# Kernel tuning notes

Measured on AMD Instinct MI355X. Metric: run time of the kernel, lower is better.

## Reference

```python
import jax, jax.numpy as jnp
import numpy as np

T, NP, NA, NV = 8, 16000, 16000, 200
DIN, H, KA, L = 256, 256, 4, 5
YEARS_TRAIN = (5, 6, 7)
BETA, EPS = 0.5, 1.0
SQRT2 = 1.4142135623730951


def setup_inputs() -> dict:
    key = jax.random.key(0)
    ks = jax.random.split(key, 24)
    s = 0.05
    return {
        'x_paper': jax.random.normal(ks[0], (T, NP, DIN), jnp.float32),
        'x_author': jax.random.normal(ks[1], (T, NA, DIN), jnp.float32),
        'x_venue': jax.random.normal(ks[2], (T, NV, DIN), jnp.float32),
        'neigh_author_idx': jax.random.randint(ks[3], (NP, KA), 0, NA),
        'neigh_venue_idx': jax.random.randint(ks[4], (NP,), 0, NV),
        'y_true': jax.random.uniform(ks[5], (len(YEARS_TRAIN), NP, L), jnp.float32, 0.0, 50.0),
        'W_paper': s * jax.random.normal(ks[6], (DIN, H), jnp.float32),
        'b_paper': jnp.zeros((H,), jnp.float32),
        'W_author': s * jax.random.normal(ks[7], (DIN, H), jnp.float32),
        'b_author': jnp.zeros((H,), jnp.float32),
        'W_venue': s * jax.random.normal(ks[8], (DIN, H), jnp.float32),
        'b_venue': jnp.zeros((H,), jnp.float32),
        'w_meta': jax.random.normal(ks[9], (3,), jnp.float32),
        'Wx': s * jax.random.normal(ks[10], (H, 3 * H), jnp.float32),
        'Wh': s * jax.random.normal(ks[11], (H, 3 * H), jnp.float32),
        'b_gru': jnp.zeros((3 * H,), jnp.float32),
        'W_eta': s * jax.random.normal(ks[12], (H, 1), jnp.float32),
        'b_eta': jnp.zeros((1,), jnp.float32),
        'W_mu': s * jax.random.normal(ks[13], (H, 1), jnp.float32),
        'b_mu': jnp.zeros((1,), jnp.float32),
        'W_sigma': s * jax.random.normal(ks[14], (H, 1), jnp.float32),
        'b_sigma': jnp.zeros((1,), jnp.float32),
    }


def reference(x_paper, x_author, x_venue, neigh_author_idx, neigh_venue_idx, y_true,
              W_paper, b_paper, W_author, b_author, W_venue, b_venue, w_meta,
              Wx, Wh, b_gru, W_eta, b_eta, W_mu, b_mu, W_sigma, b_sigma):
    # --- encoder: per-type linear + ReLU over all T snapshots ---
    emb_p = jax.nn.relu(jnp.einsum('tnd,dh->tnh', x_paper, W_paper) + b_paper)   # [T,NP,H]
    emb_a = jax.nn.relu(jnp.einsum('tnd,dh->tnh', x_author, W_author) + b_author)  # [T,NA,H]
    emb_v = jax.nn.relu(jnp.einsum('tnd,dh->tnh', x_venue, W_venue) + b_venue)   # [T,NV,H]

    # --- temporal smoothing regulariser L_time (all nodes common across years) ---
    l_time = jnp.mean(jnp.stack([
        jnp.mean(jnp.sum((e[1:] - e[:-1]) ** 2, axis=-1)) for e in (emb_p, emb_a, emb_v)
    ]))

    # --- weighted imputer, batched over all papers and all years ---
    w = jax.nn.softmax(w_meta)
    auth_mean = jnp.mean(emb_a[:, neigh_author_idx], axis=2)   # [T,NP,H]
    ven = emb_v[:, neigh_venue_idx]                            # [T,NP,H]
    v_all = w[0] * auth_mean + w[1] * ven + w[2] * emb_p       # [T,NP,H]

    # --- build lookback sequences V_p for all train years at once ---
    yrs = np.array([[t - k for k in range(1, L + 1)] for t in YEARS_TRAIN])  # [3,L]
    V = jnp.transpose(v_all[yrs], (0, 2, 1, 3)).reshape(-1, L, H)  # [B=3*NP, L, H]
    B = V.shape[0]

    # --- ImpactRNN: GRU over the lookback sequence ---
    def gru_step(h, x):
        gx = x @ Wx + b_gru
        gh = h @ Wh
        xr, xz, xn = jnp.split(gx, 3, axis=-1)
        hr, hz, hn = jnp.split(gh, 3, axis=-1)
        r = jax.nn.sigmoid(xr + hr)
        z = jax.nn.sigmoid(xz + hz)
        n = jnp.tanh(xn + r * hn)
        return (1.0 - z) * n + z * h, None

    h0 = jnp.zeros((B, H), V.dtype)
    h_last, _ = jax.lax.scan(gru_step, h0, jnp.swapaxes(V, 0, 1))

    eta = jax.nn.softplus(h_last @ W_eta + b_eta)              # [B,1]
    mu = h_last @ W_mu + b_mu                                  # [B,1]
    sigma = jax.nn.softplus(h_last @ W_sigma + b_sigma) + 1e-3  # [B,1]

    # --- cumulative log-normal citation curve, then per-horizon increments ---
    horizons = jnp.arange(1.0, L + 1.0, dtype=V.dtype)
    zscore = (jnp.log(horizons)[None, :] - mu) / (sigma * SQRT2)
    y_cum = eta * 0.5 * (1.0 + jax.lax.erf(zscore))            # [B,L]
    y_hat = jnp.concatenate([y_cum[:, :1], y_cum[:, 1:] - y_cum[:, :-1]], axis=1)

    l_pred = jnp.mean((jnp.log1p(y_true.reshape(-1, L) + EPS) - jnp.log1p(y_hat)) ** 2)
    return l_pred + BETA * l_time
```

## Files before the change

### kernel.cpp

```cpp
#include <hip/hip_runtime.h>
#include <cmath>

#define NP  16000
#define NV  200
#define HH  256

typedef short short8 __attribute__((ext_vector_type(8)));
typedef float f32x4  __attribute__((ext_vector_type(4)));

__device__ __forceinline__ unsigned short f2b(float f) {
  union { float f; unsigned u; } x; x.f = f;
  unsigned r = x.u + 0x7fffu + ((x.u >> 16) & 1u);
  return (unsigned short)(r >> 16);
}
__device__ __forceinline__ float b2f(unsigned short h) {
  union { unsigned u; float f; } x; x.u = ((unsigned)h) << 16;
  return x.f;
}
__device__ __forceinline__ float b2f_lo(unsigned u) {
  union { unsigned v; float f; } x; x.v = u << 16; return x.f;
}
__device__ __forceinline__ float b2f_hi(unsigned u) {
  union { unsigned v; float f; } x; x.v = u & 0xffff0000u; return x.f;
}
__device__ __forceinline__ unsigned cvt2(float a, float b) {
  unsigned r;
  asm("v_cvt_pk_bf16_f32 %0, %1, %2" : "=v"(r) : "v"(a), "v"(b));
  return r;
}
__device__ __forceinline__ void gld16(const void* g, void* l) {
  __builtin_amdgcn_global_load_lds((const __attribute__((address_space(1))) void*)g,
                                   (__attribute__((address_space(3))) void*)l, 16, 0, 0);
}
__device__ __forceinline__ float sigm(float x) { return 1.f / (1.f + __expf(-x)); }
__device__ __forceinline__ float tanhfast(float x) {
  const float e = __expf(-2.f * fabsf(x));
  const float t = (1.f - e) / (1.f + e);
  return x < 0.f ? -t : t;
}
__device__ __forceinline__ int xcd_swz(int orig, int q, int r) {
  const int xcd = orig & 7, loc = orig >> 3;
  return (xcd < r ? xcd * (q + 1) : r * (q + 1) + (xcd - r) * q) + loc;
}

__global__ __launch_bounds__(256) void packWt(const float* __restrict__ W,
                                              unsigned short* __restrict__ Wt) {
  const int n = blockIdx.x, k = threadIdx.x;
  Wt[n * 256 + k] = f2b(W[k * 256 + n]);
}
__global__ __launch_bounds__(256) void packW2t(const float* __restrict__ Wx,
                                               const float* __restrict__ Wh,
                                               unsigned short* __restrict__ W2t) {
  const int col = blockIdx.x;
  for (int k = threadIdx.x; k < 512; k += 256)
    W2t[(size_t)col * 512 + k] =
        f2b(k < 256 ? Wx[(size_t)k * 768 + col] : Wh[(size_t)(k - 256) * 768 + col]);
}

__global__ __launch_bounds__(512) void embed_all(
    const float* __restrict__ Xp, const float* __restrict__ Xa, const float* __restrict__ Xv,
    const unsigned short* __restrict__ Wtp, const unsigned short* __restrict__ Wta,
    const unsigned short* __restrict__ Wtv,
    const float* __restrict__ bp, const float* __restrict__ ba, const float* __restrict__ bvn,
    unsigned short* __restrict__ Ep, unsigned short* __restrict__ Ea,
    unsigned short* __restrict__ Ev) {
  __shared__ __align__(16) unsigned short lds[20480];
  unsigned short* As = lds;
  unsigned short* Bs = lds + 4096;
  const int t = threadIdx.x, w = t >> 6, l = t & 63;
  const int bid = blockIdx.x;
  const float* Xf; const unsigned short* Wt; const float* bias; unsigned short* E;
  int m0;
  if (bid < 2000)      { Xf = Xp; Wt = Wtp; bias = bp;  E = Ep; m0 = bid * 64; }
  else if (bid < 4000) { Xf = Xa; Wt = Wta; bias = ba;  E = Ea; m0 = (bid - 2000) * 64; }
  else                 { Xf = Xv; Wt = Wtv; bias = bvn; E = Ev; m0 = (bid - 4000) * 64; }
  const int srow = l >> 3, scol = ((l & 7) ^ srow) * 8;
  const int wrow = (w >> 2) * 32, wcol = (w & 3) * 64;
  const int arow = t >> 3, aseg = t & 7;
  const float* aptr = Xf + (size_t)(m0 + arow) * 256 + aseg * 8;

  f32x4 acc[2][4];
#pragma unroll
  for (int i = 0; i < 2; ++i)
#pragma unroll
    for (int j = 0; j < 4; ++j) acc[i][j] = {0.f, 0.f, 0.f, 0.f};

  float4 a0 = *reinterpret_cast<const float4*>(aptr);
  float4 a1 = *reinterpret_cast<const float4*>(aptr + 4);

#pragma unroll
  for (int c = 0; c < 4; ++c) {
#pragma unroll
    for (int i = 0; i < 4; ++i) {
      const int seg = 4 * w + i;
      gld16(Wt + (size_t)(8 * seg + srow) * 256 + c * 64 + scol, (void*)(Bs + seg * 512));
    }
    {
      uint4 u;
      u.x = cvt2(a0.x, a0.y); u.y = cvt2(a0.z, a0.w);
      u.z = cvt2(a1.x, a1.y); u.w = cvt2(a1.z, a1.w);
      const int slot = aseg ^ (arow & 7);
      *reinterpret_cast<uint4*>(As + arow * 64 + slot * 8) = u;
    }
    if (c < 3) {
      const float* np = aptr + (c + 1) * 64;
      a0 = *reinterpret_cast<const float4*>(np);
      a1 = *reinterpret_cast<const float4*>(np + 4);
    }
    __syncthreads();
#pragma unroll
    for (int ks = 0; ks < 2; ++ks) {
      short8 av[2], bv[4];
#pragma unroll
      for (int mi = 0; mi < 2; ++mi) {
        const int r = wrow + mi * 16 + (l & 15);
        const int slot = (ks * 4 + (l >> 4)) ^ (r & 7);
        av[mi] = *reinterpret_cast<const short8*>(As + r * 64 + slot * 8);
      }
#pragma unroll
      for (int nj = 0; nj < 4; ++nj) {
        const int r = wcol + nj * 16 + (l & 15);
        const int slot = (ks * 4 + (l >> 4)) ^ (r & 7);
        bv[nj] = *reinterpret_cast<const short8*>(Bs + r * 64 + slot * 8);
      }
#pragma unroll
      for (int mi = 0; mi < 2; ++mi)
#pragma unroll
        for (int nj = 0; nj < 4; ++nj)
          acc[mi][nj] = __builtin_amdgcn_mfma_f32_16x16x32_bf16(av[mi], bv[nj], acc[mi][nj], 0, 0, 0);
    }
    __syncthreads();
  }

#pragma unroll
  for (int nj = 0; nj < 4; ++nj) {
    const int col = wcol + nj * 16 + (l & 15);
    const float bvv = bias[col];
#pragma unroll
    for (int mi = 0; mi < 2; ++mi)
#pragma unroll
      for (int e = 0; e < 4; ++e) {
        const int row = wrow + mi * 16 + (l >> 4) * 4 + e;
        lds[row * 264 + col] = f2b(fmaxf(acc[mi][nj][e] + bvv, 0.f));
      }
  }
  __syncthreads();
  {
    const int r2 = t >> 3, s2 = t & 7;
    const unsigned short* src = lds + r2 * 264 + s2 * 32;
    const uint4 v0 = *reinterpret_cast<const uint4*>(src);
    const uint4 v1 = *reinterpret_cast<const uint4*>(src + 8);
    const uint4 v2 = *reinterpret_cast<const uint4*>(src + 16);
    const uint4 v3 = *reinterpret_cast<const uint4*>(src + 24);
    uint4* dst = reinterpret_cast<uint4*>(E + (size_t)(m0 + r2) * 256 + s2 * 32);
    dst[0] = v0; dst[1] = v1; dst[2] = v2; dst[3] = v3;
  }
}

__global__ __launch_bounds__(512) void gx_gemm(const unsigned short* __restrict__ Abf,
                                               const unsigned short* __restrict__ W2t,
                                               const float* __restrict__ bias,
                                               unsigned short* __restrict__ GX) {
  __shared__ __align__(16) unsigned short lds[20480];
  unsigned short* As = lds;
  unsigned short* Bs = lds + 4096;
  const int t = threadIdx.x, w = t >> 6, l = t & 63;
  const int work = xcd_swz(blockIdx.x, 656, 2);
  const int m0 = (work / 3) * 64, n0 = (work % 3) * 256;
  const int srow = l >> 3, scol = ((l & 7) ^ srow) * 8;
  const int wrow = (w >> 2) * 32, wcol = (w & 3) * 64;

  f32x4 acc[2][4];
#pragma unroll
  for (int i = 0; i < 2; ++i)
#pragma unroll
    for (int j = 0; j < 4; ++j) acc[i][j] = {0.f, 0.f, 0.f, 0.f};

#pragma unroll
  for (int c = 0; c < 4; ++c) {
    gld16(Abf + (size_t)(m0 + 8 * w + srow) * 256 + c * 64 + scol, (void*)(As + w * 512));
#pragma unroll
    for (int i = 0; i < 4; ++i) {
      const int seg = 4 * w + i;
      gld16(W2t + (size_t)(n0 + 8 * seg + srow) * 512 + c * 64 + scol, (void*)(Bs + seg * 512));
    }
    __syncthreads();
#pragma unroll
    for (int ks = 0; ks < 2; ++ks) {
      short8 av[2], bv[4];
#pragma unroll
      for (int mi = 0; mi < 2; ++mi) {
        const int r = wrow + mi * 16 + (l & 15);
        const int slot = (ks * 4 + (l >> 4)) ^ (r & 7);
        av[mi] = *reinterpret_cast<const short8*>(As + r * 64 + slot * 8);
      }
#pragma unroll
      for (int nj = 0; nj < 4; ++nj) {
        const int r = wcol + nj * 16 + (l & 15);
        const int slot = (ks * 4 + (l >> 4)) ^ (r & 7);
        bv[nj] = *reinterpret_cast<const short8*>(Bs + r * 64 + slot * 8);
      }
#pragma unroll
      for (int mi = 0; mi < 2; ++mi)
#pragma unroll
        for (int nj = 0; nj < 4; ++nj)
          acc[mi][nj] = __builtin_amdgcn_mfma_f32_16x16x32_bf16(av[mi], bv[nj], acc[mi][nj], 0, 0, 0);
    }
    __syncthreads();
  }

#pragma unroll
  for (int nj = 0; nj < 4; ++nj) {
    const int col = wcol + nj * 16 + (l & 15);
    const float bvv = bias[n0 + col];
#pragma unroll
    for (int mi = 0; mi < 2; ++mi)
#pragma unroll
      for (int e = 0; e < 4; ++e) {
        const int row = wrow + mi * 16 + (l >> 4) * 4 + e;
        lds[row * 264 + col] = f2b(acc[mi][nj][e] + bvv);
      }
  }
  __syncthreads();
  {
    const int r2 = t >> 3, s2 = t & 7;
    const unsigned short* src = lds + r2 * 264 + s2 * 32;
    const uint4 v0 = *reinterpret_cast<const uint4*>(src);
    const uint4 v1 = *reinterpret_cast<const uint4*>(src + 8);
    const uint4 v2 = *reinterpret_cast<const uint4*>(src + 16);
    const uint4 v3 = *reinterpret_cast<const uint4*>(src + 24);
    uint4* dst = reinterpret_cast<uint4*>(GX + (size_t)(m0 + r2) * 768 + n0 + s2 * 32);
    dst[0] = v0; dst[1] = v1; dst[2] = v2; dst[3] = v3;
  }
}

__global__ __launch_bounds__(256) void ltime_kernel(const unsigned short* __restrict__ ep,
                                                    const unsigned short* __restrict__ ea,
                                                    const unsigned short* __restrict__ ev,
                                                    float* __restrict__ partials) {
  const unsigned PO = 3584000u, VO = 44800u;
  const unsigned TOT = 2u * PO + VO;
  const unsigned SL = 512000u, SLV = 6400u;
  const float wbig = 1.f / (3.f * 7.f * 16000.f);
  const float wsmall = 1.f / (3.f * 7.f * 200.f);
  float local = 0.f;
  for (unsigned i = blockIdx.x * 256u + threadIdx.x; i < TOT; i += gridDim.x * 256u) {
    const unsigned short* base; unsigned off, sl; float wgt;
    if (i < 2u * PO) { base = (i < PO) ? ep : ea; off = (i < PO) ? i : i - PO; sl = SL; wgt = wbig; }
    else             { base = ev; off = i - 2u * PO; sl = SLV; wgt = wsmall; }
    const uint4 u0 = *reinterpret_cast<const uint4*>(base + (size_t)off * 8);
    const uint4 u1 = *reinterpret_cast<const uint4*>(base + (size_t)(off + sl) * 8);
    float s = 0.f, d;
    d = b2f_lo(u1.x) - b2f_lo(u0.x); s += d * d;
    d = b2f_hi(u1.x) - b2f_hi(u0.x); s += d * d;
    d = b2f_lo(u1.y) - b2f_lo(u0.y); s += d * d;
    d = b2f_hi(u1.y) - b2f_hi(u0.y); s += d * d;
    d = b2f_lo(u1.z) - b2f_lo(u0.z); s += d * d;
    d = b2f_hi(u1.z) - b2f_hi(u0.z); s += d * d;
    d = b2f_lo(u1.w) - b2f_lo(u0.w); s += d * d;
    d = b2f_hi(u1.w) - b2f_hi(u0.w); s += d * d;
    local += wgt * s;
  }
  __shared__ float red[256];
  red[threadIdx.x] = local;
  __syncthreads();
  for (int s = 128; s > 0; s >>= 1) {
    if (threadIdx.x < s) red[threadIdx.x] += red[threadIdx.x + s];
    __syncthreads();
  }
  if (threadIdx.x == 0) partials[blockIdx.x] = red[0];
}

__global__ __launch_bounds__(256) void vall_kernel(const unsigned short* __restrict__ ep,
                                                   const unsigned short* __restrict__ ea,
                                                   const unsigned short* __restrict__ ev,
                                                   const int* __restrict__ aidx,
                                                   const int* __restrict__ vidx,
                                                   const float* __restrict__ wm,
                                                   unsigned short* __restrict__ vall) {
  const int w = threadIdx.x >> 6, l = threadIdx.x & 63;
  const int n = blockIdx.x * 4 + w;
  float w0 = wm[0], w1 = wm[1], w2 = wm[2];
  const float mx = fmaxf(w0, fmaxf(w1, w2));
  const float e0 = expf(w0 - mx), e1 = expf(w1 - mx), e2 = expf(w2 - mx);
  const float inv = 1.f / (e0 + e1 + e2);
  w0 = e0 * inv; w1 = e1 * inv; w2 = e2 * inv;
  const int a0 = aidx[n * 4 + 0], a1 = aidx[n * 4 + 1];
  const int a2 = aidx[n * 4 + 2], a3 = aidx[n * 4 + 3];
  const int vn = vidx[n];
  const int cb = l * 4;
  for (int t = 0; t < 7; ++t) {
    const size_t tb = (size_t)t * NP * HH;
    const uint2 ua0 = *reinterpret_cast<const uint2*>(ea + tb + (size_t)a0 * HH + cb);
    const uint2 ua1 = *reinterpret_cast<const uint2*>(ea + tb + (size_t)a1 * HH + cb);
    const uint2 ua2 = *reinterpret_cast<const uint2*>(ea + tb + (size_t)a2 * HH + cb);
    const uint2 ua3 = *reinterpret_cast<const uint2*>(ea + tb + (size_t)a3 * HH + cb);
    const uint2 uv  = *reinterpret_cast<const uint2*>(ev + (size_t)t * NV * HH + (size_t)vn * HH + cb);
    const uint2 up  = *reinterpret_cast<const uint2*>(ep + tb + (size_t)n * HH + cb);
    float o[4];
    o[0] = w0 * 0.25f * (b2f_lo(ua0.x) + b2f_lo(ua1.x) + b2f_lo(ua2.x) + b2f_lo(ua3.x)) + w1 * b2f_lo(uv.x) + w2 * b2f_lo(up.x);
    o[1] = w0 * 0.25f * (b2f_hi(ua0.x) + b2f_hi(ua1.x) + b2f_hi(ua2.x) + b2f_hi(ua3.x)) + w1 * b2f_hi(uv.x) + w2 * b2f_hi(up.x);
    o[2] = w0 * 0.25f * (b2f_lo(ua0.y) + b2f_lo(ua1.y) + b2f_lo(ua2.y) + b2f_lo(ua3.y)) + w1 * b2f_lo(uv.y) + w2 * b2f_lo(up.y);
    o[3] = w0 * 0.25f * (b2f_hi(ua0.y) + b2f_hi(ua1.y) + b2f_hi(ua2.y) + b2f_hi(ua3.y)) + w1 * b2f_hi(uv.y) + w2 * b2f_hi(up.y);
    uint2 ov; ov.x = cvt2(o[0], o[1]); ov.y = cvt2(o[2], o[3]);
    *reinterpret_cast<uint2*>(vall + tb + (size_t)n * HH + cb) = ov;
  }
}

__global__ __launch_bounds__(256) void gru_h0(const unsigned short* __restrict__ GX,
                                              unsigned short* __restrict__ H0) {
  const int idx = blockIdx.x * 256 + threadIdx.x;
  const int hrow = idx >> 6, jq = idx & 63;
  const int g = (hrow >= 32000) ? 2 : (hrow >= 16000 ? 1 : 0);
  const int n = hrow - g * 16000;
  const size_t gxrow = (size_t)(4 + g) * 16000 + n;
  const unsigned short* gp = GX + gxrow * 768 + jq * 4;
  const uint2 uz = *reinterpret_cast<const uint2*>(gp + 256);
  const uint2 un = *reinterpret_cast<const uint2*>(gp + 512);
  float h[4];
  h[0] = (1.f - sigm(b2f_lo(uz.x))) * tanhfast(b2f_lo(un.x));
  h[1] = (1.f - sigm(b2f_hi(uz.x))) * tanhfast(b2f_hi(un.x));
  h[2] = (1.f - sigm(b2f_lo(uz.y))) * tanhfast(b2f_lo(un.y));
  h[3] = (1.f - sigm(b2f_hi(uz.y))) * tanhfast(b2f_hi(un.y));
  uint2 o; o.x = cvt2(h[0], h[1]); o.y = cvt2(h[2], h[3]);
  *reinterpret_cast<uint2*>(H0 + (size_t)hrow * 256 + jq * 4) = o;
}

__global__ __launch_bounds__(512, 2) void gru_hstep(const unsigned short* __restrict__ GX,
                                                    const unsigned short* __restrict__ W2t,
                                                    const unsigned short* __restrict__ Hsrc,
                                                    unsigned short* __restrict__ Hdst,
                                                    int lstep) {
  __shared__ __align__(16) unsigned short lds[32768];
  unsigned short* As = lds;
  unsigned short* Bs = lds + 8192;
  const int t = threadIdx.x, w = t >> 6, l = t & 63;
  const int work = xcd_swz(blockIdx.x, 93, 6);
  const int bx = work >> 1, jb = work & 1;
  const int m0 = bx * 128, j0 = jb * 128;
  const int g = bx / 125;
  const size_t gxRowBase = (size_t)(4 + g - lstep) * 16000 + (size_t)(m0 - g * 16000);
  const int srow = l >> 3;
  const int scol = ((l & 7) ^ srow) * 8;
  const int wr = w >> 2, wj = w & 3;
  f32x4 acc[3][4][2];
#pragma unroll
  for (int gate = 0; gate < 3; ++gate)
#pragma unroll
    for (int mi = 0; mi < 4; ++mi)
#pragma unroll
      for (int nj = 0; nj < 2; ++nj) acc[gate][mi][nj] = {0.f, 0.f, 0.f, 0.f};

#pragma unroll
  for (int c = 0; c < 4; ++c) {
#pragma unroll
    for (int i = 0; i < 2; ++i) {
      const int seg = w * 2 + i;
      gld16(Hsrc + (size_t)(m0 + 8 * seg + srow) * 256 + c * 64 + scol, (void*)(As + seg * 512));
    }
#pragma unroll
    for (int i = 0; i < 6; ++i) {
      const int seg = w * 6 + i;
      const int tilerow = 8 * seg + srow;
      const int gate = tilerow >> 7, jj = tilerow & 127;
      gld16(W2t + (size_t)(gate * 256 + j0 + jj) * 512 + 256 + c * 64 + scol,
            (void*)(Bs + seg * 512));
    }
    __syncthreads();
#pragma unroll
    for (int ks = 0; ks < 2; ++ks) {
      short8 av[4];
#pragma unroll
      for (int mi = 0; mi < 4; ++mi) {
        const int r = wr * 64 + mi * 16 + (l & 15);
        const int slot = (ks * 4 + (l >> 4)) ^ (r & 7);
        av[mi] = *reinterpret_cast<const short8*>(As + r * 64 + slot * 8);
      }
#pragma unroll
      for (int gate = 0; gate < 3; ++gate) {
        short8 bv0, bv1;
        {
          const int r0 = gate * 128 + wj * 32 + (l & 15);
          const int s0 = (ks * 4 + (l >> 4)) ^ (r0 & 7);
          bv0 = *reinterpret_cast<const short8*>(Bs + r0 * 64 + s0 * 8);
          const int r1 = r0 + 16;
          const int s1 = (ks * 4 + (l >> 4)) ^ (r1 & 7);
          bv1 = *reinterpret_cast<const short8*>(Bs + r1 * 64 + s1 * 8);
        }
#pragma unroll
        for (int mi = 0; mi < 4; ++mi) {
          acc[gate][mi][0] = __builtin_amdgcn_mfma_f32_16x16x32_bf16(av[mi], bv0, acc[gate][mi][0], 0, 0, 0);
          acc[gate][mi][1] = __builtin_amdgcn_mfma_f32_16x16x32_bf16(av[mi], bv1, acc[gate][mi][1], 0, 0, 0);
        }
      }
    }
    __syncthreads();
  }
  unsigned short* ep = lds + w * 2560;
#pragma unroll
  for (int nj = 0; nj < 2; ++nj) {
    const int jcol = j0 + wj * 32 + nj * 16 + (l & 15);
#pragma unroll
    for (int mi = 0; mi < 4; ++mi) {
#pragma unroll
      for (int e = 0; e < 4; ++e) {
        const int rib = wr * 64 + mi * 16 + (l >> 4) * 4 + e;
        const size_t hidx = (size_t)(m0 + rib) * 256 + jcol;
        const size_t gxoff = (gxRowBase + rib) * 768 + jcol;
        const float aR = acc[0][mi][nj][e] + b2f(GX[gxoff]);
        const float aZ = acc[1][mi][nj][e] + b2f(GX[gxoff + 256]);
        const float hn = acc[2][mi][nj][e];
        const float xn = b2f(GX[gxoff + 512]);
        const float rg = sigm(aR);
        const float zg = sigm(aZ);
        const float ng = tanhfast(xn + rg * hn);
        const float ho = b2f(Hsrc[hidx]);
        const int rl = mi * 16 + (l >> 4) * 4 + e;
        ep[rl * 40 + nj * 16 + (l & 15)] = f2b((1.f - zg) * ng + zg * ho);
      }
    }
  }
  __syncthreads();
  {
    const int grow = m0 + wr * 64 + l;
#pragma unroll
    for (int j = 0; j < 4; ++j) {
      const uint4 v = *reinterpret_cast<const uint4*>(ep + l * 40 + j * 8);
      *reinterpret_cast<uint4*>(Hdst + (size_t)grow * 256 + j0 + wj * 32 + j * 8) = v;
    }
  }
}

__device__ inline float softplusf(float x) { return x > 20.f ? x : log1pf(expf(x)); }

__global__ __launch_bounds__(256) void head_kernel(const unsigned short* __restrict__ Hbuf,
                                                   const float* __restrict__ We, const float* __restrict__ be,
                                                   const float* __restrict__ Wm, const float* __restrict__ bmu,
                                                   const float* __restrict__ Ws, const float* __restrict__ bsg,
                                                   const float* __restrict__ yt,
                                                   float* __restrict__ partials) {
  __shared__ float sWe[256], sWm[256], sWs[256];
  const int t = threadIdx.x;
  sWe[t] = We[t]; sWm[t] = Wm[t]; sWs[t] = Ws[t];
  __syncthreads();
  const int row = blockIdx.x * 256 + t;
  float loss = 0.f;
  if (row < 48000) {
    const unsigned short* h = Hbuf + (size_t)row * HH;
    float pe = 0.f, pm = 0.f, ps = 0.f;
#pragma unroll 4
    for (int k0 = 0; k0 < 256; k0 += 8) {
      const uint4 u = *reinterpret_cast<const uint4*>(h + k0);
      const float hv[8] = {b2f_lo(u.x), b2f_hi(u.x), b2f_lo(u.y), b2f_hi(u.y),
                           b2f_lo(u.z), b2f_hi(u.z), b2f_lo(u.w), b2f_hi(u.w)};
#pragma unroll
      for (int q = 0; q < 8; ++q) {
        const int k = k0 + q;
        pe += hv[q] * sWe[k]; pm += hv[q] * sWm[k]; ps += hv[q] * sWs[k];
      }
    }
    const float eta = softplusf(pe + be[0]);
    const float mu  = pm + bmu[0];
    const float sg  = softplusf(ps + bsg[0]) + 0.001f;
    const float inv = 1.f / (sg * 1.41421356237309515f);
    float prev = 0.f;
#pragma unroll
    for (int hz = 1; hz <= 5; ++hz) {
      const float z  = (logf((float)hz) - mu) * inv;
      const float yc = eta * 0.5f * (1.f + erff(z));
      const float yh = yc - prev; prev = yc;
      const float d  = log1pf(yt[(size_t)row * 5 + (hz - 1)] + 1.0f) - log1pf(yh);
      loss += d * d;
    }
  }
  __shared__ float red[256];
  red[t] = loss;
  __syncthreads();
  for (int s = 128; s > 0; s >>= 1) {
    if (t < s) red[t] += red[t + s];
    __syncthreads();
  }
  if (t == 0) partials[blockIdx.x] = red[0];
}

__global__ __launch_bounds__(256) void final_kernel(const float* __restrict__ lt,
                                                    const float* __restrict__ lp,
                                                    float* __restrict__ out) {
  __shared__ float r1[256], r2[256];
  float s1 = 0.f, s2 = 0.f;
  for (int i = threadIdx.x; i < 1024; i += 256) s1 += lt[i];
  for (int i = threadIdx.x; i < 188; i += 256) s2 += lp[i];
  r1[threadIdx.x] = s1; r2[threadIdx.x] = s2;
  __syncthreads();
  for (int s = 128; s > 0; s >>= 1) {
    if (threadIdx.x < s) { r1[threadIdx.x] += r1[threadIdx.x + s]; r2[threadIdx.x] += r2[threadIdx.x + s]; }
    __syncthreads();
  }
  if (threadIdx.x == 0) out[0] = r2[0] / 240000.f + 0.5f * r1[0];
}

extern "C" void kernel_launch(void* const* d_in, const int* in_sizes, int n_in,
                              void* d_out, int out_size, void* d_ws, size_t ws_size,
                              hipStream_t stream) {
  (void)in_sizes; (void)n_in; (void)out_size; (void)ws_size;
  const float* x_paper  = (const float*)d_in[0];
  const float* x_author = (const float*)d_in[1];
  const float* x_venue  = (const float*)d_in[2];
  const int*   aidx     = (const int*)d_in[3];
  const int*   vidx     = (const int*)d_in[4];
  const float* y_true   = (const float*)d_in[5];
  const float* W_paper  = (const float*)d_in[6];
  const float* b_paper  = (const float*)d_in[7];
  const float* W_author = (const float*)d_in[8];
  const float* b_author = (const float*)d_in[9];
  const float* W_venue  = (const float*)d_in[10];
  const float* b_venue  = (const float*)d_in[11];
  const float* w_meta   = (const float*)d_in[12];
  const float* Wx       = (const float*)d_in[13];
  const float* Wh       = (const float*)d_in[14];
  const float* b_gru    = (const float*)d_in[15];
  const float* W_eta    = (const float*)d_in[16];
  const float* b_eta    = (const float*)d_in[17];
  const float* W_mu     = (const float*)d_in[18];
  const float* b_mu     = (const float*)d_in[19];
  const float* W_sigma  = (const float*)d_in[20];
  const float* b_sigma  = (const float*)d_in[21];

  unsigned short* p = (unsigned short*)d_ws;
  unsigned short* va16 = p;  p += (size_t)7 * NP * 256;
  unsigned short* Hb0  = p;  p += (size_t)48000 * 256;
  unsigned short* Hb1  = p;  p += (size_t)48000 * 256;
  unsigned short* W2t  = p;  p += (size_t)768 * 512;
  unsigned short* GX   = p;  p += (size_t)112000 * 768;
  float* ltp = (float*)p;
  float* lpp = ltp + 1024;
  unsigned short* ep16 = GX;
  unsigned short* ea16 = ep16 + (size_t)8 * NP * 256;
  unsigned short* ev16 = ea16 + (size_t)8 * NP * 256;
  unsigned short* Wtp  = ev16 + (size_t)8 * NV * 256;
  unsigned short* Wta  = Wtp + 65536;
  unsigned short* Wtv  = Wta + 65536;

  packWt<<<256, 256, 0, stream>>>(W_paper,  Wtp);
  packWt<<<256, 256, 0, stream>>>(W_author, Wta);
  packWt<<<256, 256, 0, stream>>>(W_venue,  Wtv);
  packW2t<<<768, 256, 0, stream>>>(Wx, Wh, W2t);

  embed_all<<<4025, 512, 0, stream>>>(x_paper, x_author, x_venue, Wtp, Wta, Wtv,
                                      b_paper, b_author, b_venue, ep16, ea16, ev16);

  ltime_kernel<<<1024, 256, 0, stream>>>(ep16, ea16, ev16, ltp);
  vall_kernel<<<NP / 4, 256, 0, stream>>>(ep16, ea16, ev16, aidx, vidx, w_meta, va16);

  gx_gemm<<<5250, 512, 0, stream>>>(va16, W2t, b_gru, GX);

  gru_h0<<<12000, 256, 0, stream>>>(GX, Hb0);
  gru_hstep<<<750, 512, 0, stream>>>(GX, W2t, Hb0, Hb1, 1);
  gru_hstep<<<750, 512, 0, stream>>>(GX, W2t, Hb1, Hb0, 2);
  gru_hstep<<<750, 512, 0, stream>>>(GX, W2t, Hb0, Hb1, 3);
  gru_hstep<<<750, 512, 0, stream>>>(GX, W2t, Hb1, Hb0, 4);

  head_kernel<<<188, 256, 0, stream>>>(Hb0, W_eta, b_eta, W_mu, b_mu, W_sigma, b_sigma,
                                       y_true, lpp);
  final_kernel<<<1, 256, 0, stream>>>(ltp, lpp, (float*)d_out);
}
```

Measured before the change: 558.7 us.

## Fuse GRU recurrence steps and output head into one persistent kernel

Replaces the h0 kernel, four per-step GRU kernels and the head kernel with one kernel in which each block owns 64 rows and keeps its hidden state in LDS across all five steps. Each step reloads the Wh slice into LDS, computes all three gates with MFMA, stages the gate pre-activations through LDS and updates h in place. The head (eta, mu, sigma, loss) then runs directly from LDS. This removes the global round-trips of H, several launches and the separate head pass. In exchange the kernel uses about 130KB of LDS, so only one block fits per CU, and each 64-row block re-reads the full Wh at every step.

```diff
diff --git a/kernel.cpp b/kernel.cpp
--- a/kernel.cpp
+++ b/kernel.cpp
@@ -307,161 +307,155 @@
   }
 }
 
-__global__ __launch_bounds__(256) void gru_h0(const unsigned short* __restrict__ GX,
-                                              unsigned short* __restrict__ H0) {
-  const int idx = blockIdx.x * 256 + threadIdx.x;
-  const int hrow = idx >> 6, jq = idx & 63;
-  const int g = (hrow >= 32000) ? 2 : (hrow >= 16000 ? 1 : 0);
-  const int n = hrow - g * 16000;
-  const size_t gxrow = (size_t)(4 + g) * 16000 + n;
-  const unsigned short* gp = GX + gxrow * 768 + jq * 4;
-  const uint2 uz = *reinterpret_cast<const uint2*>(gp + 256);
-  const uint2 un = *reinterpret_cast<const uint2*>(gp + 512);
-  float h[4];
-  h[0] = (1.f - sigm(b2f_lo(uz.x))) * tanhfast(b2f_lo(un.x));
-  h[1] = (1.f - sigm(b2f_hi(uz.x))) * tanhfast(b2f_hi(un.x));
-  h[2] = (1.f - sigm(b2f_lo(uz.y))) * tanhfast(b2f_lo(un.y));
-  h[3] = (1.f - sigm(b2f_hi(uz.y))) * tanhfast(b2f_hi(un.y));
-  uint2 o; o.x = cvt2(h[0], h[1]); o.y = cvt2(h[2], h[3]);
-  *reinterpret_cast<uint2*>(H0 + (size_t)hrow * 256 + jq * 4) = o;
-}
-
-__global__ __launch_bounds__(512, 2) void gru_hstep(const unsigned short* __restrict__ GX,
-                                                    const unsigned short* __restrict__ W2t,
-                                                    const unsigned short* __restrict__ Hsrc,
-                                                    unsigned short* __restrict__ Hdst,
-                                                    int lstep) {
-  __shared__ __align__(16) unsigned short lds[32768];
-  unsigned short* As = lds;
-  unsigned short* Bs = lds + 8192;
+__global__ __launch_bounds__(512) void gru_all(
+    const unsigned short* __restrict__ GX,
+    const unsigned short* __restrict__ W2t,
+    const float* __restrict__ We, const float* __restrict__ be,
+    const float* __restrict__ Wm, const float* __restrict__ bmu,
+    const float* __restrict__ Ws, const float* __restrict__ bsg,
+    const float* __restrict__ yt,
+    float* __restrict__ partials) {
+  __shared__ __align__(16) unsigned short lds[66048];
+  __shared__ float red[512];
+  unsigned short* Hl = lds;
+  unsigned short* Bg = lds + 16384;
   const int t = threadIdx.x, w = t >> 6, l = t & 63;
-  const int work = xcd_swz(blockIdx.x, 93, 6);
-  const int bx = work >> 1, jb = work & 1;
-  const int m0 = bx * 128, j0 = jb * 128;
-  const int g = bx / 125;
-  const size_t gxRowBase = (size_t)(4 + g - lstep) * 16000 + (size_t)(m0 - g * 16000);
-  const int srow = l >> 3;
-  const int scol = ((l & 7) ^ srow) * 8;
-  const int wr = w >> 2, wj = w & 3;
-  f32x4 acc[3][4][2];
-#pragma unroll
-  for (int gate = 0; gate < 3; ++gate)
-#pragma unroll
-    for (int mi = 0; mi < 4; ++mi)
-#pragma unroll
-      for (int nj = 0; nj < 2; ++nj) acc[gate][mi][nj] = {0.f, 0.f, 0.f, 0.f};
-
-#pragma unroll
-  for (int c = 0; c < 4; ++c) {
-#pragma unroll
-    for (int i = 0; i < 2; ++i) {
-      const int seg = w * 2 + i;
-      gld16(Hsrc + (size_t)(m0 + 8 * seg + srow) * 256 + c * 64 + scol, (void*)(As + seg * 512));
-    }
-#pragma unroll
-    for (int i = 0; i < 6; ++i) {
-      const int seg = w * 6 + i;
-      const int tilerow = 8 * seg + srow;
-      const int gate = tilerow >> 7, jj = tilerow & 127;
-      gld16(W2t + (size_t)(gate * 256 + j0 + jj) * 512 + 256 + c * 64 + scol,
-            (void*)(Bs + seg * 512));
-    }
-    __syncthreads();
-#pragma unroll
-    for (int ks = 0; ks < 2; ++ks) {
-      short8 av[4];
-#pragma unroll
-      for (int mi = 0; mi < 4; ++mi) {
-        const int r = wr * 64 + mi * 16 + (l & 15);
-        const int slot = (ks * 4 + (l >> 4)) ^ (r & 7);
-        av[mi] = *reinterpret_cast<const short8*>(As + r * 64 + slot * 8);
-      }
-#pragma unroll
-      for (int gate = 0; gate < 3; ++gate) {
-        short8 bv0, bv1;
-        {
-          const int r0 = gate * 128 + wj * 32 + (l & 15);
-          const int s0 = (ks * 4 + (l >> 4)) ^ (r0 & 7);
-          bv0 = *reinterpret_cast<const short8*>(Bs + r0 * 64 + s0 * 8);
-          const int r1 = r0 + 16;
-          const int s1 = (ks * 4 + (l >> 4)) ^ (r1 & 7);
-          bv1 = *reinterpret_cast<const short8*>(Bs + r1 * 64 + s1 * 8);
+  const int m0 = blockIdx.x * 64;
+  const int g = m0 / 16000;
+  const int nloc = m0 - g * 16000;
+  const int srow = l >> 3, scol = ((l & 7) ^ srow) * 8;
+  const int wm = w >> 2, wn = w & 3;
+  const int crow = t >> 3, cseg = t & 7;
+
+  for (int step = 0; step < 5; ++step) {
+    const size_t gxBase = (size_t)(4 + g - step) * 16000 + nloc;
+    if (step > 0) {
+      f32x4 acc[2][12];
+#pragma unroll
+      for (int mi = 0; mi < 2; ++mi)
+#pragma unroll
+        for (int nj = 0; nj < 12; ++nj) acc[mi][nj] = {0.f, 0.f, 0.f, 0.f};
+
+      for (int c = 0; c < 4; ++c) {
+#pragma unroll
+        for (int i = 0; i < 12; ++i) {
+          const int seg = w * 12 + i;
+          const int br = 8 * seg + srow;
+          const int jj = br / 3, gate = br - 3 * jj;
+          gld16(W2t + (size_t)(gate * 256 + jj) * 512 + 256 + c * 64 + scol,
+                (void*)(Bg + seg * 512));
         }
-#pragma unroll
-        for (int mi = 0; mi < 4; ++mi) {
-          acc[gate][mi][0] = __builtin_amdgcn_mfma_f32_16x16x32_bf16(av[mi], bv0, acc[gate][mi][0], 0, 0, 0);
-          acc[gate][mi][1] = __builtin_amdgcn_mfma_f32_16x16x32_bf16(av[mi], bv1, acc[gate][mi][1], 0, 0, 0);
+        __syncthreads();
+#pragma unroll
+        for (int ks = 0; ks < 2; ++ks) {
+          short8 av[2];
+#pragma unroll
+          for (int mi = 0; mi < 2; ++mi) {
+            const int r = wm * 32 + mi * 16 + (l & 15);
+            const int slot = (ks * 4 + (l >> 4)) ^ (r & 7);
+            av[mi] = *reinterpret_cast<const short8*>(Hl + c * 4096 + r * 64 + slot * 8);
+          }
+#pragma unroll
+          for (int nj = 0; nj < 12; ++nj) {
+            const int br = wn * 192 + nj * 16 + (l & 15);
+            const int slot = (ks * 4 + (l >> 4)) ^ (br & 7);
+            const short8 bv = *reinterpret_cast<const short8*>(Bg + br * 64 + slot * 8);
+            acc[0][nj] = __builtin_amdgcn_mfma_f32_16x16x32_bf16(av[0], bv, acc[0][nj], 0, 0, 0);
+            acc[1][nj] = __builtin_amdgcn_mfma_f32_16x16x32_bf16(av[1], bv, acc[1][nj], 0, 0, 0);
+          }
         }
-      }
-    }
-    __syncthreads();
-  }
-  unsigned short* ep = lds + w * 2560;
-#pragma unroll
-  for (int nj = 0; nj < 2; ++nj) {
-    const int jcol = j0 + wj * 32 + nj * 16 + (l & 15);
-#pragma unroll
-    for (int mi = 0; mi < 4; ++mi) {
-#pragma unroll
-      for (int e = 0; e < 4; ++e) {
-        const int rib = wr * 64 + mi * 16 + (l >> 4) * 4 + e;
-        const size_t hidx = (size_t)(m0 + rib) * 256 + jcol;
-        const size_t gxoff = (gxRowBase + rib) * 768 + jcol;
-        const float aR = acc[0][mi][nj][e] + b2f(GX[gxoff]);
-        const float aZ = acc[1][mi][nj][e] + b2f(GX[gxoff + 256]);
-        const float hn = acc[2][mi][nj][e];
-        const float xn = b2f(GX[gxoff + 512]);
-        const float rg = sigm(aR);
-        const float zg = sigm(aZ);
-        const float ng = tanhfast(xn + rg * hn);
-        const float ho = b2f(Hsrc[hidx]);
-        const int rl = mi * 16 + (l >> 4) * 4 + e;
-        ep[rl * 40 + nj * 16 + (l & 15)] = f2b((1.f - zg) * ng + zg * ho);
-      }
-    }
-  }
+        __syncthreads();
+      }
+#pragma unroll
+      for (int nj = 0; nj < 12; ++nj) {
+        const int br = wn * 192 + nj * 16 + (l & 15);
+#pragma unroll
+        for (int mi = 0; mi < 2; ++mi)
+#pragma unroll
+          for (int e = 0; e < 4; ++e) {
+            const int row = wm * 32 + mi * 16 + (l >> 4) * 4 + e;
+            Bg[row * 776 + br] = f2b(acc[mi][nj][e]);
+          }
+      }
+      __syncthreads();
+    }
+
+    {
+      const unsigned short* gxp = GX + (gxBase + crow) * 768;
+      const int hc = cseg >> 1;
+#pragma unroll
+      for (int qq = 0; qq < 4; ++qq) {
+        const int j0 = cseg * 32 + qq * 8;
+        const int ls = (cseg & 1) * 4 + qq;
+        unsigned short* hp = Hl + hc * 4096 + crow * 64 + (ls ^ (crow & 7)) * 8;
+        const uint4 uz = *reinterpret_cast<const uint4*>(gxp + 256 + j0);
+        const uint4 un = *reinterpret_cast<const uint4*>(gxp + 512 + j0);
+        float xz[8], xn[8];
+        xz[0]=b2f_lo(uz.x); xz[1]=b2f_hi(uz.x); xz[2]=b2f_lo(uz.y); xz[3]=b2f_hi(uz.y);
+        xz[4]=b2f_lo(uz.z); xz[5]=b2f_hi(uz.z); xz[6]=b2f_lo(uz.w); xz[7]=b2f_hi(uz.w);
+        xn[0]=b2f_lo(un.x); xn[1]=b2f_hi(un.x); xn[2]=b2f_lo(un.y); xn[3]=b2f_hi(un.y);
+        xn[4]=b2f_lo(un.z); xn[5]=b2f_hi(un.z); xn[6]=b2f_lo(un.w); xn[7]=b2f_hi(un.w);
+        float hnew[8];
+        if (step == 0) {
+#pragma unroll
+          for (int e2 = 0; e2 < 8; ++e2)
+            hnew[e2] = (1.f - sigm(xz[e2])) * tanhfast(xn[e2]);
+        } else {
+          const uint4 ur = *reinterpret_cast<const uint4*>(gxp + j0);
+          float xr[8];
+          xr[0]=b2f_lo(ur.x); xr[1]=b2f_hi(ur.x); xr[2]=b2f_lo(ur.y); xr[3]=b2f_hi(ur.y);
+          xr[4]=b2f_lo(ur.z); xr[5]=b2f_hi(ur.z); xr[6]=b2f_lo(ur.w); xr[7]=b2f_hi(ur.w);
+          const uint4 ho = *reinterpret_cast<const uint4*>(hp);
+          float hold[8];
+          hold[0]=b2f_lo(ho.x); hold[1]=b2f_hi(ho.x); hold[2]=b2f_lo(ho.y); hold[3]=b2f_hi(ho.y);
+          hold[4]=b2f_lo(ho.z); hold[5]=b2f_hi(ho.z); hold[6]=b2f_lo(ho.w); hold[7]=b2f_hi(ho.w);
+          const unsigned short* gl = Bg + crow * 776 + 3 * j0;
+#pragma unroll
+          for (int e2 = 0; e2 < 8; ++e2) {
+            const float hr = b2f(gl[3 * e2 + 0]);
+            const float hz = b2f(gl[3 * e2 + 1]);
+            const float hn = b2f(gl[3 * e2 + 2]);
+            const float rg = sigm(hr + xr[e2]);
+            const float zg = sigm(hz + xz[e2]);
+            const float ng = tanhfast(xn[e2] + rg * hn);
+            hnew[e2] = (1.f - zg) * ng + zg * hold[e2];
+          }
+        }
+        uint4 o;
+        o.x = cvt2(hnew[0], hnew[1]); o.y = cvt2(hnew[2], hnew[3]);
+        o.z = cvt2(hnew[4], hnew[5]); o.w = cvt2(hnew[6], hnew[7]);
+        *reinterpret_cast<uint4*>(hp) = o;
+      }
+    }
+    __syncthreads();
+  }
+
+  float* gf = (float*)Bg;
+  if (t < 256) { gf[t] = We[t]; gf[256 + t] = Wm[t]; gf[512 + t] = Ws[t]; }
   __syncthreads();
-  {
-    const int grow = m0 + wr * 64 + l;
-#pragma unroll
-    for (int j = 0; j < 4; ++j) {
-      const uint4 v = *reinterpret_cast<const uint4*>(ep + l * 40 + j * 8);
-      *reinterpret_cast<uint4*>(Hdst + (size_t)grow * 256 + j0 + wj * 32 + j * 8) = v;
-    }
-  }
-}
-
-__device__ inline float softplusf(float x) { return x > 20.f ? x : log1pf(expf(x)); }
-
-__global__ __launch_bounds__(256) void head_kernel(const unsigned short* __restrict__ Hbuf,
-                                                   const float* __restrict__ We, const float* __restrict__ be,
-                                                   const float* __restrict__ Wm, const float* __restrict__ bmu,
-                                                   const float* __restrict__ Ws, const float* __restrict__ bsg,
-                                                   const float* __restrict__ yt,
-                                                   float* __restrict__ partials) {
-  __shared__ float sWe[256], sWm[256], sWs[256];
-  const int t = threadIdx.x;
-  sWe[t] = We[t]; sWm[t] = Wm[t]; sWs[t] = Ws[t];
-  __syncthreads();
-  const int row = blockIdx.x * 256 + t;
   float loss = 0.f;
-  if (row < 48000) {
-    const unsigned short* h = Hbuf + (size_t)row * HH;
+  if (t < 64) {
+    const int row = t;
     float pe = 0.f, pm = 0.f, ps = 0.f;
-#pragma unroll 4
-    for (int k0 = 0; k0 < 256; k0 += 8) {
-      const uint4 u = *reinterpret_cast<const uint4*>(h + k0);
-      const float hv[8] = {b2f_lo(u.x), b2f_hi(u.x), b2f_lo(u.y), b2f_hi(u.y),
-                           b2f_lo(u.z), b2f_hi(u.z), b2f_lo(u.w), b2f_hi(u.w)};
-#pragma unroll
-      for (int q = 0; q < 8; ++q) {
-        const int k = k0 + q;
-        pe += hv[q] * sWe[k]; pm += hv[q] * sWm[k]; ps += hv[q] * sWs[k];
-      }
-    }
-    const float eta = softplusf(pe + be[0]);
+#pragma unroll
+    for (int c = 0; c < 4; ++c)
+#pragma unroll
+      for (int s = 0; s < 8; ++s) {
+        const uint4 u = *reinterpret_cast<const uint4*>(
+            Hl + c * 4096 + row * 64 + (s ^ (row & 7)) * 8);
+        const float hv[8] = {b2f_lo(u.x), b2f_hi(u.x), b2f_lo(u.y), b2f_hi(u.y),
+                             b2f_lo(u.z), b2f_hi(u.z), b2f_lo(u.w), b2f_hi(u.w)};
+#pragma unroll
+        for (int q = 0; q < 8; ++q) {
+          const int k = c * 64 + s * 8 + q;
+          pe += hv[q] * gf[k]; pm += hv[q] * gf[256 + k]; ps += hv[q] * gf[512 + k];
+        }
+      }
+    const float x1 = pe + be[0];
+    const float eta = x1 > 20.f ? x1 : log1pf(expf(x1));
     const float mu  = pm + bmu[0];
-    const float sg  = softplusf(ps + bsg[0]) + 0.001f;
+    const float x2 = ps + bsg[0];
+    const float sg  = (x2 > 20.f ? x2 : log1pf(expf(x2))) + 0.001f;
     const float inv = 1.f / (sg * 1.41421356237309515f);
     float prev = 0.f;
 #pragma unroll
@@ -469,14 +463,13 @@
       const float z  = (logf((float)hz) - mu) * inv;
       const float yc = eta * 0.5f * (1.f + erff(z));
       const float yh = yc - prev; prev = yc;
-      const float d  = log1pf(yt[(size_t)row * 5 + (hz - 1)] + 1.0f) - log1pf(yh);
+      const float d  = log1pf(yt[(size_t)(m0 + row) * 5 + (hz - 1)] + 1.0f) - log1pf(yh);
       loss += d * d;
     }
   }
-  __shared__ float red[256];
   red[t] = loss;
   __syncthreads();
-  for (int s = 128; s > 0; s >>= 1) {
+  for (int s = 256; s > 0; s >>= 1) {
     if (t < s) red[t] += red[t + s];
     __syncthreads();
   }
@@ -489,7 +482,7 @@
   __shared__ float r1[256], r2[256];
   float s1 = 0.f, s2 = 0.f;
   for (int i = threadIdx.x; i < 1024; i += 256) s1 += lt[i];
-  for (int i = threadIdx.x; i < 188; i += 256) s2 += lp[i];
+  for (int i = threadIdx.x; i < 750; i += 256) s2 += lp[i];
   r1[threadIdx.x] = s1; r2[threadIdx.x] = s2;
   __syncthreads();
   for (int s = 128; s > 0; s >>= 1) {
@@ -528,8 +521,6 @@
 
   unsigned short* p = (unsigned short*)d_ws;
   unsigned short* va16 = p;  p += (size_t)7 * NP * 256;
-  unsigned short* Hb0  = p;  p += (size_t)48000 * 256;
-  unsigned short* Hb1  = p;  p += (size_t)48000 * 256;
   unsigned short* W2t  = p;  p += (size_t)768 * 512;
   unsigned short* GX   = p;  p += (size_t)112000 * 768;
   float* ltp = (float*)p;
@@ -554,13 +545,8 @@
 
   gx_gemm<<<5250, 512, 0, stream>>>(va16, W2t, b_gru, GX);
 
-  gru_h0<<<12000, 256, 0, stream>>>(GX, Hb0);
-  gru_hstep<<<750, 512, 0, stream>>>(GX, W2t, Hb0, Hb1, 1);
-  gru_hstep<<<750, 512, 0, stream>>>(GX, W2t, Hb1, Hb0, 2);
-  gru_hstep<<<750, 512, 0, stream>>>(GX, W2t, Hb0, Hb1, 3);
-  gru_hstep<<<750, 512, 0, stream>>>(GX, W2t, Hb1, Hb0, 4);
-
-  head_kernel<<<188, 256, 0, stream>>>(Hb0, W_eta, b_eta, W_mu, b_mu, W_sigma, b_sigma,
-                                       y_true, lpp);
+  gru_all<<<750, 512, 0, stream>>>(GX, W2t, W_eta, b_eta, W_mu, b_mu,
+                                   W_sigma, b_sigma, y_true, lpp);
+
   final_kernel<<<1, 256, 0, stream>>>(ltp, lpp, (float*)d_out);
 }
```

New measurement: 706.4 us. 26.4% more time.

## Load GEMM operands directly from global into registers, merge weight pack kernels

Applied to the files above, without the earlier changes.

The embed and gx GEMM kernels stop staging A and B tiles through LDS with barriers. Each wave now loads its MFMA fragments straight from global memory into registers, converting fp32 to bf16 inline for the embed input. This removes LDS round-trips and __syncthreads. The cost is redundant global and L2 traffic, since tiles are no longer shared across waves, and less coalesced loads. Separately, the four weight-pack launches are fused into one kernel to cut launch overhead.

```diff
diff --git a/kernel.cpp b/kernel.cpp
--- a/kernel.cpp
+++ b/kernel.cpp
@@ -43,18 +43,27 @@
   return (xcd < r ? xcd * (q + 1) : r * (q + 1) + (xcd - r) * q) + loc;
 }
 
-__global__ __launch_bounds__(256) void packWt(const float* __restrict__ W,
-                                              unsigned short* __restrict__ Wt) {
-  const int n = blockIdx.x, k = threadIdx.x;
-  Wt[n * 256 + k] = f2b(W[k * 256 + n]);
-}
-__global__ __launch_bounds__(256) void packW2t(const float* __restrict__ Wx,
-                                               const float* __restrict__ Wh,
-                                               unsigned short* __restrict__ W2t) {
-  const int col = blockIdx.x;
-  for (int k = threadIdx.x; k < 512; k += 256)
-    W2t[(size_t)col * 512 + k] =
-        f2b(k < 256 ? Wx[(size_t)k * 768 + col] : Wh[(size_t)(k - 256) * 768 + col]);
+__global__ __launch_bounds__(256) void pack_all(const float* __restrict__ Wp,
+                                                const float* __restrict__ Wa,
+                                                const float* __restrict__ Wv,
+                                                const float* __restrict__ Wx,
+                                                const float* __restrict__ Wh,
+                                                unsigned short* __restrict__ Wtp,
+                                                unsigned short* __restrict__ Wta,
+                                                unsigned short* __restrict__ Wtv,
+                                                unsigned short* __restrict__ W2t) {
+  const int b = blockIdx.x, k = threadIdx.x;
+  if (b < 768) {
+    const float* W = b < 256 ? Wp : (b < 512 ? Wa : Wv);
+    unsigned short* Wt = b < 256 ? Wtp : (b < 512 ? Wta : Wtv);
+    const int n = b & 255;
+    Wt[n * 256 + k] = f2b(W[k * 256 + n]);
+  } else {
+    const int col = b - 768;
+    for (int kk = k; kk < 512; kk += 256)
+      W2t[(size_t)col * 512 + kk] =
+          f2b(kk < 256 ? Wx[(size_t)kk * 768 + col] : Wh[(size_t)(kk - 256) * 768 + col]);
+  }
 }
 
 __global__ __launch_bounds__(512) void embed_all(
@@ -64,9 +73,7 @@
     const float* __restrict__ bp, const float* __restrict__ ba, const float* __restrict__ bvn,
     unsigned short* __restrict__ Ep, unsigned short* __restrict__ Ea,
     unsigned short* __restrict__ Ev) {
-  __shared__ __align__(16) unsigned short lds[20480];
-  unsigned short* As = lds;
-  unsigned short* Bs = lds + 4096;
+  __shared__ __align__(16) unsigned short lds[16896];
   const int t = threadIdx.x, w = t >> 6, l = t & 63;
   const int bid = blockIdx.x;
   const float* Xf; const unsigned short* Wt; const float* bias; unsigned short* E;
@@ -74,10 +81,8 @@
   if (bid < 2000)      { Xf = Xp; Wt = Wtp; bias = bp;  E = Ep; m0 = bid * 64; }
   else if (bid < 4000) { Xf = Xa; Wt = Wta; bias = ba;  E = Ea; m0 = (bid - 2000) * 64; }
   else                 { Xf = Xv; Wt = Wtv; bias = bvn; E = Ev; m0 = (bid - 4000) * 64; }
-  const int srow = l >> 3, scol = ((l & 7) ^ srow) * 8;
   const int wrow = (w >> 2) * 32, wcol = (w & 3) * 64;
-  const int arow = t >> 3, aseg = t & 7;
-  const float* aptr = Xf + (size_t)(m0 + arow) * 256 + aseg * 8;
+  const int lr = l & 15, lk = (l >> 4) * 8;
 
   f32x4 acc[2][4];
 #pragma unroll
@@ -85,56 +90,43 @@
 #pragma unroll
     for (int j = 0; j < 4; ++j) acc[i][j] = {0.f, 0.f, 0.f, 0.f};
 
-  float4 a0 = *reinterpret_cast<const float4*>(aptr);
-  float4 a1 = *reinterpret_cast<const float4*>(aptr + 4);
-
 #pragma unroll
   for (int c = 0; c < 4; ++c) {
-#pragma unroll
-    for (int i = 0; i < 4; ++i) {
-      const int seg = 4 * w + i;
-      gld16(Wt + (size_t)(8 * seg + srow) * 256 + c * 64 + scol, (void*)(Bs + seg * 512));
-    }
-    {
-      uint4 u;
-      u.x = cvt2(a0.x, a0.y); u.y = cvt2(a0.z, a0.w);
-      u.z = cvt2(a1.x, a1.y); u.w = cvt2(a1.z, a1.w);
-      const int slot = aseg ^ (arow & 7);
-      *reinterpret_cast<uint4*>(As + arow * 64 + slot * 8) = u;
-    }
-    if (c < 3) {
-      const float* np = aptr + (c + 1) * 64;
-      a0 = *reinterpret_cast<const float4*>(np);
-      a1 = *reinterpret_cast<const float4*>(np + 4);
-    }
-    __syncthreads();
-#pragma unroll
-    for (int ks = 0; ks < 2; ++ks) {
-      short8 av[2], bv[4];
+    const int k0 = c * 64;
+    short8 bv[2][4];
+#pragma unroll
+    for (int ks = 0; ks < 2; ++ks)
+#pragma unroll
+      for (int nj = 0; nj < 4; ++nj) {
+        const int col = wcol + nj * 16 + lr;
+        bv[ks][nj] = *reinterpret_cast<const short8*>(Wt + (size_t)col * 256 + k0 + ks * 32 + lk);
+      }
+    short8 av[2][2];
+#pragma unroll
+    for (int ks = 0; ks < 2; ++ks)
 #pragma unroll
       for (int mi = 0; mi < 2; ++mi) {
-        const int r = wrow + mi * 16 + (l & 15);
-        const int slot = (ks * 4 + (l >> 4)) ^ (r & 7);
-        av[mi] = *reinterpret_cast<const short8*>(As + r * 64 + slot * 8);
-      }
-#pragma unroll
-      for (int nj = 0; nj < 4; ++nj) {
-        const int r = wcol + nj * 16 + (l & 15);
-        const int slot = (ks * 4 + (l >> 4)) ^ (r & 7);
-        bv[nj] = *reinterpret_cast<const short8*>(Bs + r * 64 + slot * 8);
-      }
+        const int row = wrow + mi * 16 + lr;
+        const float* ap = Xf + (size_t)(m0 + row) * 256 + k0 + ks * 32 + lk;
+        const float4 f0 = *reinterpret_cast<const float4*>(ap);
+        const float4 f1 = *reinterpret_cast<const float4*>(ap + 4);
+        union { unsigned u[4]; short8 s8; } cv;
+        cv.u[0] = cvt2(f0.x, f0.y); cv.u[1] = cvt2(f0.z, f0.w);
+        cv.u[2] = cvt2(f1.x, f1.y); cv.u[3] = cvt2(f1.z, f1.w);
+        av[ks][mi] = cv.s8;
+      }
+#pragma unroll
+    for (int ks = 0; ks < 2; ++ks)
 #pragma unroll
       for (int mi = 0; mi < 2; ++mi)
 #pragma unroll
         for (int nj = 0; nj < 4; ++nj)
-          acc[mi][nj] = __builtin_amdgcn_mfma_f32_16x16x32_bf16(av[mi], bv[nj], acc[mi][nj], 0, 0, 0);
-    }
-    __syncthreads();
+          acc[mi][nj] = __builtin_amdgcn_mfma_f32_16x16x32_bf16(av[ks][mi], bv[ks][nj], acc[mi][nj], 0, 0, 0);
   }
 
 #pragma unroll
   for (int nj = 0; nj < 4; ++nj) {
-    const int col = wcol + nj * 16 + (l & 15);
+    const int col = wcol + nj * 16 + lr;
     const float bvv = bias[col];
 #pragma unroll
     for (int mi = 0; mi < 2; ++mi)
@@ -161,14 +153,12 @@
                                                const unsigned short* __restrict__ W2t,
                                                const float* __restrict__ bias,
                                                unsigned short* __restrict__ GX) {
-  __shared__ __align__(16) unsigned short lds[20480];
-  unsigned short* As = lds;
-  unsigned short* Bs = lds + 4096;
+  __shared__ __align__(16) unsigned short lds[16896];
   const int t = threadIdx.x, w = t >> 6, l = t & 63;
   const int work = xcd_swz(blockIdx.x, 656, 2);
   const int m0 = (work / 3) * 64, n0 = (work % 3) * 256;
-  const int srow = l >> 3, scol = ((l & 7) ^ srow) * 8;
   const int wrow = (w >> 2) * 32, wcol = (w & 3) * 64;
+  const int lr = l & 15, lk = (l >> 4) * 8;
 
   f32x4 acc[2][4];
 #pragma unroll
@@ -178,40 +168,35 @@
 
 #pragma unroll
   for (int c = 0; c < 4; ++c) {
-    gld16(Abf + (size_t)(m0 + 8 * w + srow) * 256 + c * 64 + scol, (void*)(As + w * 512));
-#pragma unroll
-    for (int i = 0; i < 4; ++i) {
-      const int seg = 4 * w + i;
-      gld16(W2t + (size_t)(n0 + 8 * seg + srow) * 512 + c * 64 + scol, (void*)(Bs + seg * 512));
-    }
-    __syncthreads();
-#pragma unroll
-    for (int ks = 0; ks < 2; ++ks) {
-      short8 av[2], bv[4];
+    const int k0 = c * 64;
+    short8 bv[2][4];
+#pragma unroll
+    for (int ks = 0; ks < 2; ++ks)
+#pragma unroll
+      for (int nj = 0; nj < 4; ++nj) {
+        const int col = n0 + wcol + nj * 16 + lr;
+        bv[ks][nj] = *reinterpret_cast<const short8*>(W2t + (size_t)col * 512 + k0 + ks * 32 + lk);
+      }
+    short8 av[2][2];
+#pragma unroll
+    for (int ks = 0; ks < 2; ++ks)
 #pragma unroll
       for (int mi = 0; mi < 2; ++mi) {
-        const int r = wrow + mi * 16 + (l & 15);
-        const int slot = (ks * 4 + (l >> 4)) ^ (r & 7);
-        av[mi] = *reinterpret_cast<const short8*>(As + r * 64 + slot * 8);
-      }
-#pragma unroll
-      for (int nj = 0; nj < 4; ++nj) {
-        const int r = wcol + nj * 16 + (l & 15);
-        const int slot = (ks * 4 + (l >> 4)) ^ (r & 7);
-        bv[nj] = *reinterpret_cast<const short8*>(Bs + r * 64 + slot * 8);
-      }
+        const int row = wrow + mi * 16 + lr;
+        av[ks][mi] = *reinterpret_cast<const short8*>(Abf + (size_t)(m0 + row) * 256 + k0 + ks * 32 + lk);
+      }
+#pragma unroll
+    for (int ks = 0; ks < 2; ++ks)
 #pragma unroll
       for (int mi = 0; mi < 2; ++mi)
 #pragma unroll
         for (int nj = 0; nj < 4; ++nj)
-          acc[mi][nj] = __builtin_amdgcn_mfma_f32_16x16x32_bf16(av[mi], bv[nj], acc[mi][nj], 0, 0, 0);
-    }
-    __syncthreads();
+          acc[mi][nj] = __builtin_amdgcn_mfma_f32_16x16x32_bf16(av[ks][mi], bv[ks][nj], acc[mi][nj], 0, 0, 0);
   }
 
 #pragma unroll
   for (int nj = 0; nj < 4; ++nj) {
-    const int col = wcol + nj * 16 + (l & 15);
+    const int col = wcol + nj * 16 + lr;
     const float bvv = bias[n0 + col];
 #pragma unroll
     for (int mi = 0; mi < 2; ++mi)
@@ -541,10 +526,8 @@
   unsigned short* Wta  = Wtp + 65536;
   unsigned short* Wtv  = Wta + 65536;
 
-  packWt<<<256, 256, 0, stream>>>(W_paper,  Wtp);
-  packWt<<<256, 256, 0, stream>>>(W_author, Wta);
-  packWt<<<256, 256, 0, stream>>>(W_venue,  Wtv);
-  packW2t<<<768, 256, 0, stream>>>(Wx, Wh, W2t);
+  pack_all<<<1536, 256, 0, stream>>>(W_paper, W_author, W_venue, Wx, Wh,
+                                     Wtp, Wta, Wtv, W2t);
 
   embed_all<<<4025, 512, 0, stream>>>(x_paper, x_author, x_venue, Wtp, Wta, Wtv,
                                       b_paper, b_author, b_venue, ep16, ea16, ev16);
```

Result: slower. 863.9 us (+54.6%).
